# Kernel tuning notes

Hardware: AMD Instinct MI355X
Metric: run time of the kernel (lower is better)

Reference implementation:

```python
import jax, jax.numpy as jnp
import numpy as np

N = 50000
E = 800000
N_CT = 32
EMBED = 256
HIDDEN = 128
OUT = 512
NEG_SLOPE = 0.2


def setup_inputs() -> dict:
    key = jax.random.key(0)
    ks = jax.random.split(key, 12)
    ct_idx = jax.random.randint(ks[0], (N,), 0, N_CT)
    cell_type_onehot = jax.nn.one_hot(ct_idx, N_CT, dtype=jnp.float32)
    lipid_droplet_scalar = jax.random.normal(ks[1], (N,), dtype=jnp.float32)
    edge_index = jax.random.randint(ks[2], (2, E), 0, N, dtype=jnp.int32)
    s = 0.05
    return {
        "cell_type_onehot": cell_type_onehot,
        "lipid_droplet_scalar": lipid_droplet_scalar,
        "edge_index": edge_index,
        "W_embed": jax.random.normal(ks[3], (N_CT + 1, EMBED), dtype=jnp.float32) * s,
        "b_embed": jnp.zeros((EMBED,), dtype=jnp.float32),
        "W_l": jax.random.normal(ks[4], (EMBED, HIDDEN), dtype=jnp.float32) * s,
        "b_l": jnp.zeros((HIDDEN,), dtype=jnp.float32),
        "W_r": jax.random.normal(ks[5], (EMBED, HIDDEN), dtype=jnp.float32) * s,
        "b_r": jnp.zeros((HIDDEN,), dtype=jnp.float32),
        "att": jax.random.normal(ks[6], (HIDDEN,), dtype=jnp.float32) * s,
        "gat_bias": jnp.zeros((HIDDEN,), dtype=jnp.float32),
        "W_out": jax.random.normal(ks[7], (HIDDEN, OUT), dtype=jnp.float32) * s,
        "b_out": jnp.zeros((OUT,), dtype=jnp.float32),
        "dispersion": jax.random.normal(ks[8], (OUT, N_CT), dtype=jnp.float32) * s,
    }


def reference(cell_type_onehot, lipid_droplet_scalar, edge_index,
              W_embed, b_embed, W_l, b_l, W_r, b_r, att, gat_bias,
              W_out, b_out, dispersion):
    n = cell_type_onehot.shape[0]
    lds = lipid_droplet_scalar[:, None] if lipid_droplet_scalar.ndim == 1 else lipid_droplet_scalar
    combined = jnp.concatenate([cell_type_onehot, lds], axis=1)  # [N, n_ct+1]
    x = jax.nn.elu(combined @ W_embed + b_embed)  # [N, EMBED]

    # GATv2Conv, heads=1, concat=True (PyG semantics)
    x_l = x @ W_l + b_l  # source-side transform [N, H]
    x_r = x @ W_r + b_r  # target-side transform [N, H]
    src, dst = edge_index[0], edge_index[1]
    e = jax.nn.leaky_relu(x_l[src] + x_r[dst], negative_slope=NEG_SLOPE)  # [E, H]
    logit = e @ att  # [E]
    # scatter-softmax over incoming edges of each target node
    m = jax.ops.segment_max(logit, dst, num_segments=n)
    alpha = jnp.exp(logit - m[dst])
    denom = jax.ops.segment_sum(alpha, dst, num_segments=n)
    alpha = alpha / (denom[dst] + 1e-16)
    agg = jax.ops.segment_sum(alpha[:, None] * x_l[src], dst, num_segments=n)  # [N, H]
    h = jax.nn.elu(agg + gat_bias)

    logits = h @ W_out + b_out  # [N, OUT]
    ct_idx = jnp.argmax(cell_type_onehot, axis=1)  # [N]
    disp = jax.nn.softplus(dispersion[:, ct_idx]).T  # [N, OUT]
    return logits, disp
```

## Files before the change

### kernel.cpp

```cpp
#include <hip/hip_runtime.h>
#include <hip/hip_bf16.h>
#include <math.h>

#define N    50000
#define E    800000
#define NCT  32
#define EMB  256
#define HID  128
#define OUTD 512
#define NB_SCAN 49
#define XPAD 257
#define HPAD 132

__device__ __forceinline__ float4 fma4s(float a, float4 b, float4 c) {
    return make_float4(fmaf(a, b.x, c.x), fmaf(a, b.y, c.y),
                       fmaf(a, b.z, c.z), fmaf(a, b.w, c.w));
}
__device__ __forceinline__ float4 add4(float4 a, float4 b) {
    return make_float4(a.x + b.x, a.y + b.y, a.z + b.z, a.w + b.w);
}

__global__ void k_init(const float* __restrict__ onehot,
                       const float* __restrict__ dispersion,
                       int* __restrict__ ct, int* __restrict__ hist,
                       float* __restrict__ spt) {
    int i = blockIdx.x * 256 + threadIdx.x;
    if (i < N) {
        const float* row = onehot + (size_t)i * NCT;
        int c = 0;
        #pragma unroll
        for (int j = 0; j < NCT; j++)
            if (row[j] > 0.5f) c = j;
        ct[i] = c;
        hist[i] = 0;
    }
    if (i < OUTD * NCT) {
        float x = dispersion[i];
        float s = log1pf(expf(-fabsf(x))) + fmaxf(x, 0.f);
        int c = i >> 5, j = i & 31;
        spt[j * OUTD + c] = s;
    }
}

__global__ __launch_bounds__(256) void k_hist(const int* __restrict__ eidx,
                                              int* __restrict__ hist) {
    int i = blockIdx.x * 256 + threadIdx.x;
    if (i < E / 4) {
        int4 d = reinterpret_cast<const int4*>(eidx + E)[i];
        atomicAdd(&hist[d.x], 1);
        atomicAdd(&hist[d.y], 1);
        atomicAdd(&hist[d.z], 1);
        atomicAdd(&hist[d.w], 1);
    }
}

__global__ __launch_bounds__(256, 4) void k_xlr(
        const int* __restrict__ ct, const float* __restrict__ ldsc,
        const float* __restrict__ We, const float* __restrict__ be,
        const float* __restrict__ pWl, const float* __restrict__ pbl,
        const float* __restrict__ pWr, const float* __restrict__ pbr,
        float* __restrict__ xl, float* __restrict__ xr) {
    __shared__ float xs[32 * XPAD];
    __shared__ int   ctl[32];
    __shared__ float ldl[32];
    const int t  = threadIdx.x;
    const int n0 = blockIdx.x * 32;

    if (t < 32) {
        int n = n0 + t; if (n >= N) n = N - 1;
        ctl[t] = ct[n];
        ldl[t] = ldsc[n];
    }
    __syncthreads();

    {
        const float w32 = We[NCT * EMB + t];
        const float bb  = be[t];
        for (int m = 0; m < 32; m++) {
            float v = fmaf(ldl[m], w32, We[ctl[m] * EMB + t]) + bb;
            xs[m * XPAD + t] = v > 0.f ? v : expm1f(v);
        }
    }
    __syncthreads();

    const int cg = t & 31;
    const int rg = t >> 5;
    const int c  = cg * 8;
    const float* Wb = (c < HID) ? (pWl + c) : (pWr + (c - HID));
    const float* xrow = xs + rg * 4 * XPAD;

    float4 acc[4][2];
    #pragma unroll
    for (int r = 0; r < 4; r++) {
        acc[r][0] = make_float4(0.f, 0.f, 0.f, 0.f);
        acc[r][1] = make_float4(0.f, 0.f, 0.f, 0.f);
    }

    for (int k = 0; k < EMB; k += 4) {
        float4 b[4][2];
        #pragma unroll
        for (int kk = 0; kk < 4; kk++) {
            b[kk][0] = *reinterpret_cast<const float4*>(Wb + (k + kk) * HID);
            b[kk][1] = *reinterpret_cast<const float4*>(Wb + (k + kk) * HID + 4);
        }
        float a[4][4];
        #pragma unroll
        for (int kk = 0; kk < 4; kk++)
            #pragma unroll
            for (int r = 0; r < 4; r++)
                a[kk][r] = xrow[r * XPAD + k + kk];
        #pragma unroll
        for (int kk = 0; kk < 4; kk++)
            #pragma unroll
            for (int r = 0; r < 4; r++) {
                acc[r][0] = fma4s(a[kk][r], b[kk][0], acc[r][0]);
                acc[r][1] = fma4s(a[kk][r], b[kk][1], acc[r][1]);
            }
    }

    float* OutP;
    int cc;
    float4 bias0, bias1;
    if (c < HID) {
        OutP = xl; cc = c;
        bias0 = *reinterpret_cast<const float4*>(pbl + cc);
        bias1 = *reinterpret_cast<const float4*>(pbl + cc + 4);
    } else {
        OutP = xr; cc = c - HID;
        bias0 = *reinterpret_cast<const float4*>(pbr + cc);
        bias1 = *reinterpret_cast<const float4*>(pbr + cc + 4);
    }
    #pragma unroll
    for (int r = 0; r < 4; r++) {
        int n = n0 + rg * 4 + r;
        if (n < N) {
            *reinterpret_cast<float4*>(OutP + (size_t)n * HID + cc)     = add4(acc[r][0], bias0);
            *reinterpret_cast<float4*>(OutP + (size_t)n * HID + cc + 4) = add4(acc[r][1], bias1);
        }
    }
}

__global__ __launch_bounds__(1024) void k_scan1(const int* __restrict__ hist,
                                                int* __restrict__ offs,
                                                int* __restrict__ bsum) {
    __shared__ int sb[2][1024];
    const int t = threadIdx.x;
    const int i = blockIdx.x * 1024 + t;
    int v = (i < N) ? hist[i] : 0;
    sb[0][t] = v;
    __syncthreads();
    int pin = 0;
    for (int off = 1; off < 1024; off <<= 1) {
        int x = sb[pin][t];
        if (t >= off) x += sb[pin][t - off];
        sb[pin ^ 1][t] = x;
        pin ^= 1;
        __syncthreads();
    }
    int incl = sb[pin][t];
    if (i < N) offs[i] = incl - v;
    if (t == 1023) bsum[blockIdx.x] = incl;
}

__global__ void k_scan2(const int* __restrict__ bsum, int* __restrict__ bbase) {
    if (threadIdx.x == 0) {
        int run = 0;
        for (int j = 0; j < NB_SCAN; j++) { bbase[j] = run; run += bsum[j]; }
    }
}

__global__ __launch_bounds__(1024) void k_scan3(int* __restrict__ offs,
                                                int* __restrict__ cursor,
                                                const int* __restrict__ bbase) {
    const int t = threadIdx.x;
    const int i = blockIdx.x * 1024 + t;
    if (i < N) {
        int v = offs[i] + bbase[blockIdx.x];
        offs[i] = v;
        cursor[i] = v;
    }
    if (blockIdx.x == 0 && t == 0) offs[N] = E;
}

__global__ __launch_bounds__(256) void k_scatter(const int* __restrict__ eidx,
                                                 int* __restrict__ cursor,
                                                 int* __restrict__ sorted) {
    const int e = blockIdx.x * 256 + threadIdx.x;
    if (e < E) {
        int s = eidx[e];
        int d = eidx[E + e];
        int pos = atomicAdd(&cursor[d], 1);
        sorted[pos] = s;
    }
}

__global__ __launch_bounds__(256, 8) void k_agg(
        const int* __restrict__ offs, const int* __restrict__ srt,
        const float* __restrict__ xl, const float* __restrict__ attv,
        const float* __restrict__ gb, float* xrh) {
    const int t = threadIdx.x;
    const int n = blockIdx.x * 4 + (t >> 6);
    if (n >= N) return;
    const int lane = t & 63;
    const float2* xl2 = reinterpret_cast<const float2*>(xl);
    float2* xh2 = reinterpret_cast<float2*>(xrh);

    const float2 xr2 = xh2[(size_t)n * 64 + lane];
    const float2 at2 = reinterpret_cast<const float2*>(attv)[lane];
    const int i0  = offs[n];
    const int deg = offs[n + 1] - i0;

    float m = -3.0e38f, den = 0.f;
    float2 acc = make_float2(0.f, 0.f);
    float2 xnx = make_float2(0.f, 0.f);
    if (deg > 0) { int s = srt[i0]; xnx = xl2[(size_t)s * 64 + lane]; }

    for (int i = 0; i < deg; i++) {
        float2 xc = xnx;
        if (i + 1 < deg) { int s = srt[i0 + i + 1]; xnx = xl2[(size_t)s * 64 + lane]; }
        float vx = xc.x + xr2.x, vy = xc.y + xr2.y;
        vx = vx > 0.f ? vx : 0.2f * vx;
        vy = vy > 0.f ? vy : 0.2f * vy;
        float p = fmaf(vx, at2.x, vy * at2.y);
        #pragma unroll
        for (int msk = 32; msk; msk >>= 1) p += __shfl_xor(p, msk);
        if (p <= m) {
            float w = __expf(p - m);
            den += w;
            acc.x = fmaf(w, xc.x, acc.x);
            acc.y = fmaf(w, xc.y, acc.y);
        } else {
            float s = __expf(m - p);
            den = fmaf(den, s, 1.f);
            acc.x = fmaf(acc.x, s, xc.x);
            acc.y = fmaf(acc.y, s, xc.y);
            m = p;
        }
    }
    float inv = 1.f / (den + 1e-16f);
    const float2 g2 = reinterpret_cast<const float2*>(gb)[lane];
    float hx = fmaf(acc.x, inv, g2.x);
    float hy = fmaf(acc.y, inv, g2.y);
    hx = hx > 0.f ? hx : expm1f(hx);
    hy = hy > 0.f ? hy : expm1f(hy);
    xh2[(size_t)n * 64 + lane] = make_float2(hx, hy);
}

__global__ __launch_bounds__(256, 4) void k_out(
        const float* __restrict__ h, const int* __restrict__ ct,
        const float* __restrict__ Wo, const float* __restrict__ bo,
        const float* __restrict__ spt, float* __restrict__ out) {
    __shared__ float hs[32 * HPAD];
    __shared__ int ctl[32];
    const int t  = threadIdx.x;
    const int n0 = blockIdx.x * 32;

    if (t < 32) { int n = n0 + t; ctl[t] = ct[n < N ? n : N - 1]; }
    {
        const float4* h4 = reinterpret_cast<const float4*>(h);
        #pragma unroll
        for (int j = 0; j < 4; j++) {
            int idx4 = t + j * 256;
            int row  = idx4 >> 5;
            int k4   = (idx4 & 31) * 4;
            int n = n0 + row;
            float4 v = (n < N) ? h4[(size_t)n * 32 + (idx4 & 31)]
                               : make_float4(0.f, 0.f, 0.f, 0.f);
            float* d = hs + row * HPAD + k4;
            d[0] = v.x; d[1] = v.y; d[2] = v.z; d[3] = v.w;
        }
    }
    __syncthreads();

    const int cg = t & 31, rg = t >> 5;
    const float* hrow = hs + rg * 4 * HPAD;
    float* outd = out + (size_t)N * OUTD;

    for (int cp = 0; cp < 2; cp++) {
        const int c = cp * 256 + cg * 8;
        float4 acc[4][2];
        #pragma unroll
        for (int r = 0; r < 4; r++) {
            acc[r][0] = make_float4(0.f, 0.f, 0.f, 0.f);
            acc[r][1] = make_float4(0.f, 0.f, 0.f, 0.f);
        }
        for (int k = 0; k < HID; k += 4) {
            float4 b[4][2];
            #pragma unroll
            for (int kk = 0; kk < 4; kk++) {
                b[kk][0] = *reinterpret_cast<const float4*>(Wo + (k + kk) * OUTD + c);
                b[kk][1] = *reinterpret_cast<const float4*>(Wo + (k + kk) * OUTD + c + 4);
            }
            float a[4][4];
            #pragma unroll
            for (int kk = 0; kk < 4; kk++)
                #pragma unroll
                for (int r = 0; r < 4; r++)
                    a[kk][r] = hrow[r * HPAD + k + kk];
            #pragma unroll
            for (int kk = 0; kk < 4; kk++)
                #pragma unroll
                for (int r = 0; r < 4; r++) {
                    acc[r][0] = fma4s(a[kk][r], b[kk][0], acc[r][0]);
                    acc[r][1] = fma4s(a[kk][r], b[kk][1], acc[r][1]);
                }
        }
        float4 bias0 = *reinterpret_cast<const float4*>(bo + c);
        float4 bias1 = *reinterpret_cast<const float4*>(bo + c + 4);
        #pragma unroll
        for (int r = 0; r < 4; r++) {
            int n = n0 + rg * 4 + r;
            if (n < N) {
                *reinterpret_cast<float4*>(out + (size_t)n * OUTD + c)     = add4(acc[r][0], bias0);
                *reinterpret_cast<float4*>(out + (size_t)n * OUTD + c + 4) = add4(acc[r][1], bias1);
                int cn = ctl[rg * 4 + r];
                float4 d0 = *reinterpret_cast<const float4*>(spt + cn * OUTD + c);
                float4 d1 = *reinterpret_cast<const float4*>(spt + cn * OUTD + c + 4);
                *reinterpret_cast<float4*>(outd + (size_t)n * OUTD + c)     = d0;
                *reinterpret_cast<float4*>(outd + (size_t)n * OUTD + c + 4) = d1;
            }
        }
    }
}

extern "C" void kernel_launch(void* const* d_in, const int* in_sizes, int n_in,
                              void* d_out, int out_size, void* d_ws, size_t ws_size,
                              hipStream_t stream) {
    const float* onehot     = (const float*)d_in[0];
    const float* ldsc       = (const float*)d_in[1];
    const int*   eidx       = (const int*)  d_in[2];
    const float* We         = (const float*)d_in[3];
    const float* be         = (const float*)d_in[4];
    const float* Wl         = (const float*)d_in[5];
    const float* bl         = (const float*)d_in[6];
    const float* Wr         = (const float*)d_in[7];
    const float* br         = (const float*)d_in[8];
    const float* attv       = (const float*)d_in[9];
    const float* gb         = (const float*)d_in[10];
    const float* Wo         = (const float*)d_in[11];
    const float* bo         = (const float*)d_in[12];
    const float* dispersion = (const float*)d_in[13];

    float* ws     = (float*)d_ws;
    float* xl     = ws;
    float* xr     = xl + (size_t)N * HID;
    int*   sorted = (int*)(xr + (size_t)N * HID);
    int*   ct     = sorted + E;
    int*   offs   = ct + N;
    int*   cursor = offs + (N + 1);
    int*   hist   = cursor + (N + 1);
    float* spt    = (float*)(hist + N);
    int*   bsum   = (int*)(spt + NCT * OUTD);
    int*   bbase  = bsum + 64;

    float* out = (float*)d_out;

    k_init   <<<(N + 255) / 256, 256, 0, stream>>>(onehot, dispersion, ct, hist, spt);
    k_hist   <<<(E / 4 + 255) / 256, 256, 0, stream>>>(eidx, hist);
    k_xlr    <<<(N + 31) / 32, 256, 0, stream>>>(ct, ldsc, We, be, Wl, bl, Wr, br, xl, xr);
    k_scan1  <<<NB_SCAN, 1024, 0, stream>>>(hist, offs, bsum);
    k_scan2  <<<1, 64, 0, stream>>>(bsum, bbase);
    k_scan3  <<<NB_SCAN, 1024, 0, stream>>>(offs, cursor, bbase);
    k_scatter<<<(E + 255) / 256, 256, 0, stream>>>(eidx, cursor, sorted);
    k_agg    <<<(N + 3) / 4, 256, 0, stream>>>(offs, sorted, xl, attv, gb, xr);
    k_out    <<<(N + 31) / 32, 256, 0, stream>>>(xr, ct, Wo, bo, spt, out);
}
```

Measured before the change: 673.9 us.

## Stage weights in LDS for GEMMs and widen agg to 32-lane float4 with unrolled prefetch

```diff
diff --git a/kernel.cpp b/kernel.cpp
--- a/kernel.cpp
+++ b/kernel.cpp
@@ -9,7 +9,7 @@
 #define HID  128
 #define OUTD 512
 #define NB_SCAN 49
-#define XPAD 257
+#define XPAD 260
 #define HPAD 132
 
 __device__ __forceinline__ float4 fma4s(float a, float4 b, float4 c) {
@@ -54,13 +54,14 @@
     }
 }
 
-__global__ __launch_bounds__(256, 4) void k_xlr(
+__global__ __launch_bounds__(256, 3) void k_xlr(
         const int* __restrict__ ct, const float* __restrict__ ldsc,
         const float* __restrict__ We, const float* __restrict__ be,
         const float* __restrict__ pWl, const float* __restrict__ pbl,
         const float* __restrict__ pWr, const float* __restrict__ pbr,
         float* __restrict__ xl, float* __restrict__ xr) {
     __shared__ float xs[32 * XPAD];
+    __shared__ float Bs[16 * 256];
     __shared__ int   ctl[32];
     __shared__ float ldl[32];
     const int t  = threadIdx.x;
@@ -81,61 +82,68 @@
             xs[m * XPAD + t] = v > 0.f ? v : expm1f(v);
         }
     }
-    __syncthreads();
 
     const int cg = t & 31;
     const int rg = t >> 5;
-    const int c  = cg * 8;
-    const float* Wb = (c < HID) ? (pWl + c) : (pWr + (c - HID));
     const float* xrow = xs + rg * 4 * XPAD;
-
-    float4 acc[4][2];
+    const int cA = cg * 4;
+    const int st_kk  = t >> 6;
+    const int st_col = (t & 63) * 4;
+
+    float4 accA[4], accB[4];
     #pragma unroll
     for (int r = 0; r < 4; r++) {
-        acc[r][0] = make_float4(0.f, 0.f, 0.f, 0.f);
-        acc[r][1] = make_float4(0.f, 0.f, 0.f, 0.f);
-    }
-
-    for (int k = 0; k < EMB; k += 4) {
-        float4 b[4][2];
-        #pragma unroll
-        for (int kk = 0; kk < 4; kk++) {
-            b[kk][0] = *reinterpret_cast<const float4*>(Wb + (k + kk) * HID);
-            b[kk][1] = *reinterpret_cast<const float4*>(Wb + (k + kk) * HID + 4);
-        }
-        float a[4][4];
-        #pragma unroll
-        for (int kk = 0; kk < 4; kk++)
+        accA[r] = make_float4(0.f, 0.f, 0.f, 0.f);
+        accB[r] = make_float4(0.f, 0.f, 0.f, 0.f);
+    }
+
+    for (int kc = 0; kc < EMB; kc += 16) {
+        __syncthreads();
+        #pragma unroll
+        for (int j = 0; j < 4; j++) {
+            int kk  = st_kk + j * 4;
+            int col = st_col;
+            const float* src = (col < HID) ? (pWl + (size_t)(kc + kk) * HID + col)
+                                           : (pWr + (size_t)(kc + kk) * HID + col - HID);
+            *reinterpret_cast<float4*>(&Bs[kk * 256 + col]) =
+                *reinterpret_cast<const float4*>(src);
+        }
+        __syncthreads();
+
+        #pragma unroll
+        for (int kk = 0; kk < 16; kk += 4) {
+            float4 bA[4], bB[4];
+            #pragma unroll
+            for (int q = 0; q < 4; q++) {
+                bA[q] = *reinterpret_cast<const float4*>(&Bs[(kk + q) * 256 + cA]);
+                bB[q] = *reinterpret_cast<const float4*>(&Bs[(kk + q) * 256 + 128 + cA]);
+            }
+            float4 a[4];
             #pragma unroll
             for (int r = 0; r < 4; r++)
-                a[kk][r] = xrow[r * XPAD + k + kk];
-        #pragma unroll
-        for (int kk = 0; kk < 4; kk++)
+                a[r] = *reinterpret_cast<const float4*>(xrow + r * XPAD + kc + kk);
             #pragma unroll
             for (int r = 0; r < 4; r++) {
-                acc[r][0] = fma4s(a[kk][r], b[kk][0], acc[r][0]);
-                acc[r][1] = fma4s(a[kk][r], b[kk][1], acc[r][1]);
+                accA[r] = fma4s(a[r].x, bA[0], accA[r]);
+                accB[r] = fma4s(a[r].x, bB[0], accB[r]);
+                accA[r] = fma4s(a[r].y, bA[1], accA[r]);
+                accB[r] = fma4s(a[r].y, bB[1], accB[r]);
+                accA[r] = fma4s(a[r].z, bA[2], accA[r]);
+                accB[r] = fma4s(a[r].z, bB[2], accB[r]);
+                accA[r] = fma4s(a[r].w, bA[3], accA[r]);
+                accB[r] = fma4s(a[r].w, bB[3], accB[r]);
             }
-    }
-
-    float* OutP;
-    int cc;
-    float4 bias0, bias1;
-    if (c < HID) {
-        OutP = xl; cc = c;
-        bias0 = *reinterpret_cast<const float4*>(pbl + cc);
-        bias1 = *reinterpret_cast<const float4*>(pbl + cc + 4);
-    } else {
-        OutP = xr; cc = c - HID;
-        bias0 = *reinterpret_cast<const float4*>(pbr + cc);
-        bias1 = *reinterpret_cast<const float4*>(pbr + cc + 4);
-    }
+        }
+    }
+
+    const float4 biasA = *reinterpret_cast<const float4*>(pbl + cA);
+    const float4 biasB = *reinterpret_cast<const float4*>(pbr + cA);
     #pragma unroll
     for (int r = 0; r < 4; r++) {
         int n = n0 + rg * 4 + r;
         if (n < N) {
-            *reinterpret_cast<float4*>(OutP + (size_t)n * HID + cc)     = add4(acc[r][0], bias0);
-            *reinterpret_cast<float4*>(OutP + (size_t)n * HID + cc + 4) = add4(acc[r][1], bias1);
+            *reinterpret_cast<float4*>(xl + (size_t)n * HID + cA) = add4(accA[r], biasA);
+            *reinterpret_cast<float4*>(xr + (size_t)n * HID + cA) = add4(accB[r], biasB);
         }
     }
 }
@@ -199,58 +207,80 @@
         const float* __restrict__ xl, const float* __restrict__ attv,
         const float* __restrict__ gb, float* xrh) {
     const int t = threadIdx.x;
-    const int n = blockIdx.x * 4 + (t >> 6);
+    const int n = blockIdx.x * 8 + (t >> 5);
     if (n >= N) return;
-    const int lane = t & 63;
-    const float2* xl2 = reinterpret_cast<const float2*>(xl);
-    float2* xh2 = reinterpret_cast<float2*>(xrh);
-
-    const float2 xr2 = xh2[(size_t)n * 64 + lane];
-    const float2 at2 = reinterpret_cast<const float2*>(attv)[lane];
+    const int lane = t & 31;
+    const float4* xl4 = reinterpret_cast<const float4*>(xl);
+    float4* xh4 = reinterpret_cast<float4*>(xrh);
+
+    const float4 xr4 = xh4[(size_t)n * 32 + lane];
+    const float4 at4 = reinterpret_cast<const float4*>(attv)[lane];
     const int i0  = offs[n];
     const int deg = offs[n + 1] - i0;
 
     float m = -3.0e38f, den = 0.f;
-    float2 acc = make_float2(0.f, 0.f);
-    float2 xnx = make_float2(0.f, 0.f);
-    if (deg > 0) { int s = srt[i0]; xnx = xl2[(size_t)s * 64 + lane]; }
-
-    for (int i = 0; i < deg; i++) {
-        float2 xc = xnx;
-        if (i + 1 < deg) { int s = srt[i0 + i + 1]; xnx = xl2[(size_t)s * 64 + lane]; }
-        float vx = xc.x + xr2.x, vy = xc.y + xr2.y;
-        vx = vx > 0.f ? vx : 0.2f * vx;
-        vy = vy > 0.f ? vy : 0.2f * vy;
-        float p = fmaf(vx, at2.x, vy * at2.y);
-        #pragma unroll
-        for (int msk = 32; msk; msk >>= 1) p += __shfl_xor(p, msk);
-        if (p <= m) {
-            float w = __expf(p - m);
-            den += w;
-            acc.x = fmaf(w, xc.x, acc.x);
-            acc.y = fmaf(w, xc.y, acc.y);
-        } else {
-            float s = __expf(m - p);
-            den = fmaf(den, s, 1.f);
-            acc.x = fmaf(acc.x, s, xc.x);
-            acc.y = fmaf(acc.y, s, xc.y);
-            m = p;
-        }
-    }
+    float4 acc = make_float4(0.f, 0.f, 0.f, 0.f);
+
+#define STEP(XC) {                                                          \
+    float vx = XC.x + xr4.x, vy = XC.y + xr4.y,                             \
+          vz = XC.z + xr4.z, vw = XC.w + xr4.w;                             \
+    vx = fmaxf(vx, 0.f) + 0.2f * fminf(vx, 0.f);                            \
+    vy = fmaxf(vy, 0.f) + 0.2f * fminf(vy, 0.f);                            \
+    vz = fmaxf(vz, 0.f) + 0.2f * fminf(vz, 0.f);                            \
+    vw = fmaxf(vw, 0.f) + 0.2f * fminf(vw, 0.f);                            \
+    float p = fmaf(vx, at4.x, fmaf(vy, at4.y, fmaf(vz, at4.z, vw * at4.w)));\
+    p += __shfl_xor(p, 16); p += __shfl_xor(p, 8);                          \
+    p += __shfl_xor(p, 4);  p += __shfl_xor(p, 2); p += __shfl_xor(p, 1);   \
+    float mn = fmaxf(m, p);                                                 \
+    float sc = __expf(m - mn);                                              \
+    float w  = __expf(p - mn);                                              \
+    den   = fmaf(den, sc, w);                                               \
+    acc.x = fmaf(acc.x, sc, w * XC.x);                                      \
+    acc.y = fmaf(acc.y, sc, w * XC.y);                                      \
+    acc.z = fmaf(acc.z, sc, w * XC.z);                                      \
+    acc.w = fmaf(acc.w, sc, w * XC.w);                                      \
+    m = mn; }
+
+    if (deg > 0) {
+        const int lastI = i0 + deg - 1;
+        #define LDX(J) xl4[(size_t)srt[min(i0 + (J), lastI)] * 32 + lane]
+        float4 x0 = LDX(0), x1 = LDX(1), x2 = LDX(2), x3 = LDX(3);
+        int i = 0;
+        for (; i + 4 <= deg; i += 4) {
+            const int base = i0 + i + 4;
+            float4 n0 = xl4[(size_t)srt[min(base + 0, lastI)] * 32 + lane];
+            float4 n1 = xl4[(size_t)srt[min(base + 1, lastI)] * 32 + lane];
+            float4 n2 = xl4[(size_t)srt[min(base + 2, lastI)] * 32 + lane];
+            float4 n3 = xl4[(size_t)srt[min(base + 3, lastI)] * 32 + lane];
+            STEP(x0); STEP(x1); STEP(x2); STEP(x3);
+            x0 = n0; x1 = n1; x2 = n2; x3 = n3;
+        }
+        if (i     < deg) STEP(x0);
+        if (i + 1 < deg) STEP(x1);
+        if (i + 2 < deg) STEP(x2);
+        #undef LDX
+    }
+#undef STEP
+
     float inv = 1.f / (den + 1e-16f);
-    const float2 g2 = reinterpret_cast<const float2*>(gb)[lane];
-    float hx = fmaf(acc.x, inv, g2.x);
-    float hy = fmaf(acc.y, inv, g2.y);
+    const float4 g4 = reinterpret_cast<const float4*>(gb)[lane];
+    float hx = fmaf(acc.x, inv, g4.x);
+    float hy = fmaf(acc.y, inv, g4.y);
+    float hz = fmaf(acc.z, inv, g4.z);
+    float hw = fmaf(acc.w, inv, g4.w);
     hx = hx > 0.f ? hx : expm1f(hx);
     hy = hy > 0.f ? hy : expm1f(hy);
-    xh2[(size_t)n * 64 + lane] = make_float2(hx, hy);
-}
-
-__global__ __launch_bounds__(256, 4) void k_out(
+    hz = hz > 0.f ? hz : expm1f(hz);
+    hw = hw > 0.f ? hw : expm1f(hw);
+    xh4[(size_t)n * 32 + lane] = make_float4(hx, hy, hz, hw);
+}
+
+__global__ __launch_bounds__(256, 3) void k_out(
         const float* __restrict__ h, const int* __restrict__ ct,
         const float* __restrict__ Wo, const float* __restrict__ bo,
         const float* __restrict__ spt, float* __restrict__ out) {
     __shared__ float hs[32 * HPAD];
+    __shared__ float Bs[16 * OUTD];
     __shared__ int ctl[32];
     const int t  = threadIdx.x;
     const int n0 = blockIdx.x * 32;
@@ -270,54 +300,79 @@
             d[0] = v.x; d[1] = v.y; d[2] = v.z; d[3] = v.w;
         }
     }
-    __syncthreads();
 
     const int cg = t & 31, rg = t >> 5;
     const float* hrow = hs + rg * 4 * HPAD;
-    float* outd = out + (size_t)N * OUTD;
-
-    for (int cp = 0; cp < 2; cp++) {
-        const int c = cp * 256 + cg * 8;
-        float4 acc[4][2];
+    const int cA = cg * 4;
+    const int st_kk  = t >> 7;
+    const int st_col = (t & 127) * 4;
+
+    float4 acc[2][4][2];
+    #pragma unroll
+    for (int cp = 0; cp < 2; cp++)
         #pragma unroll
         for (int r = 0; r < 4; r++) {
-            acc[r][0] = make_float4(0.f, 0.f, 0.f, 0.f);
-            acc[r][1] = make_float4(0.f, 0.f, 0.f, 0.f);
-        }
-        for (int k = 0; k < HID; k += 4) {
-            float4 b[4][2];
+            acc[cp][r][0] = make_float4(0.f, 0.f, 0.f, 0.f);
+            acc[cp][r][1] = make_float4(0.f, 0.f, 0.f, 0.f);
+        }
+
+    for (int kc = 0; kc < HID; kc += 16) {
+        __syncthreads();
+        #pragma unroll
+        for (int j = 0; j < 8; j++) {
+            int kk = st_kk + j * 2;
+            *reinterpret_cast<float4*>(&Bs[kk * OUTD + st_col]) =
+                *reinterpret_cast<const float4*>(Wo + (size_t)(kc + kk) * OUTD + st_col);
+        }
+        __syncthreads();
+
+        #pragma unroll
+        for (int kk = 0; kk < 16; kk += 4) {
+            float4 a[4];
             #pragma unroll
-            for (int kk = 0; kk < 4; kk++) {
-                b[kk][0] = *reinterpret_cast<const float4*>(Wo + (k + kk) * OUTD + c);
-                b[kk][1] = *reinterpret_cast<const float4*>(Wo + (k + kk) * OUTD + c + 4);
-            }
-            float a[4][4];
+            for (int r = 0; r < 4; r++)
+                a[r] = *reinterpret_cast<const float4*>(hrow + r * HPAD + kc + kk);
             #pragma unroll
-            for (int kk = 0; kk < 4; kk++)
+            for (int cp = 0; cp < 2; cp++) {
+                float4 bA[4], bB[4];
                 #pragma unroll
-                for (int r = 0; r < 4; r++)
-                    a[kk][r] = hrow[r * HPAD + k + kk];
-            #pragma unroll
-            for (int kk = 0; kk < 4; kk++)
+                for (int q = 0; q < 4; q++) {
+                    bA[q] = *reinterpret_cast<const float4*>(&Bs[(kk + q) * OUTD + cp * 256 + cA]);
+                    bB[q] = *reinterpret_cast<const float4*>(&Bs[(kk + q) * OUTD + cp * 256 + 128 + cA]);
+                }
                 #pragma unroll
                 for (int r = 0; r < 4; r++) {
-                    acc[r][0] = fma4s(a[kk][r], b[kk][0], acc[r][0]);
-                    acc[r][1] = fma4s(a[kk][r], b[kk][1], acc[r][1]);
+                    acc[cp][r][0] = fma4s(a[r].x, bA[0], acc[cp][r][0]);
+                    acc[cp][r][1] = fma4s(a[r].x, bB[0], acc[cp][r][1]);
+                    acc[cp][r][0] = fma4s(a[r].y, bA[1], acc[cp][r][0]);
+                    acc[cp][r][1] = fma4s(a[r].y, bB[1], acc[cp][r][1]);
+                    acc[cp][r][0] = fma4s(a[r].z, bA[2], acc[cp][r][0]);
+                    acc[cp][r][1] = fma4s(a[r].z, bB[2], acc[cp][r][1]);
+                    acc[cp][r][0] = fma4s(a[r].w, bA[3], acc[cp][r][0]);
+                    acc[cp][r][1] = fma4s(a[r].w, bB[3], acc[cp][r][1]);
                 }
-        }
-        float4 bias0 = *reinterpret_cast<const float4*>(bo + c);
-        float4 bias1 = *reinterpret_cast<const float4*>(bo + c + 4);
+            }
+        }
+    }
+
+    float* outd = out + (size_t)N * OUTD;
+    #pragma unroll
+    for (int cp = 0; cp < 2; cp++) {
+        const int c0 = cp * 256 + cA;
+        const int c1 = cp * 256 + 128 + cA;
+        const float4 bias0 = *reinterpret_cast<const float4*>(bo + c0);
+        const float4 bias1 = *reinterpret_cast<const float4*>(bo + c1);
         #pragma unroll
         for (int r = 0; r < 4; r++) {
             int n = n0 + rg * 4 + r;
             if (n < N) {
-                *reinterpret_cast<float4*>(out + (size_t)n * OUTD + c)     = add4(acc[r][0], bias0);
-                *reinterpret_cast<float4*>(out + (size_t)n * OUTD + c + 4) = add4(acc[r][1], bias1);
+                *reinterpret_cast<float4*>(out + (size_t)n * OUTD + c0) = add4(acc[cp][r][0], bias0);
+                *reinterpret_cast<float4*>(out + (size_t)n * OUTD + c1) = add4(acc[cp][r][1], bias1);
                 int cn = ctl[rg * 4 + r];
-                float4 d0 = *reinterpret_cast<const float4*>(spt + cn * OUTD + c);
-                float4 d1 = *reinterpret_cast<const float4*>(spt + cn * OUTD + c + 4);
-                *reinterpret_cast<float4*>(outd + (size_t)n * OUTD + c)     = d0;
-                *reinterpret_cast<float4*>(outd + (size_t)n * OUTD + c + 4) = d1;
+                *reinterpret_cast<float4*>(outd + (size_t)n * OUTD + c0) =
+                    *reinterpret_cast<const float4*>(spt + cn * OUTD + c0);
+                *reinterpret_cast<float4*>(outd + (size_t)n * OUTD + c1) =
+                    *reinterpret_cast<const float4*>(spt + cn * OUTD + c1);
             }
         }
     }
@@ -362,6 +417,6 @@
     k_scan2  <<<1, 64, 0, stream>>>(bsum, bbase);
     k_scan3  <<<NB_SCAN, 1024, 0, stream>>>(offs, cursor, bbase);
     k_scatter<<<(E + 255) / 256, 256, 0, stream>>>(eidx, cursor, sorted);
-    k_agg    <<<(N + 3) / 4, 256, 0, stream>>>(offs, sorted, xl, attv, gb, xr);
+    k_agg    <<<(N + 7) / 8, 256, 0, stream>>>(offs, sorted, xl, attv, gb, xr);
     k_out    <<<(N + 31) / 32, 256, 0, stream>>>(xr, ct, Wo, bo, spt, out);
 }
```

Result: faster. 611.5 us (-9.3%).
